# Kernel optimization log

Measured on AMD Instinct MI355X. Metric: run time of the kernel, lower is better.

## Reference

```python
import jax, jax.numpy as jnp
import numpy as np

EMBED_DIM = 2048
HEAD_DIM = 128
B, T = 4, 2048


def setup_inputs() -> dict:
    key = jax.random.key(0)
    k1, k2, k3, k4 = jax.random.split(key, 4)
    x_in = jax.random.normal(k1, (B, T, EMBED_DIM), dtype=jnp.float32)
    scale = 1.0 / np.sqrt(EMBED_DIM)
    Wq = jax.random.normal(k2, (EMBED_DIM, HEAD_DIM), dtype=jnp.float32) * scale
    Wk = jax.random.normal(k3, (EMBED_DIM, HEAD_DIM), dtype=jnp.float32) * scale
    Wv = jax.random.normal(k4, (EMBED_DIM, HEAD_DIM), dtype=jnp.float32) * scale
    return {"x_in": x_in, "Wq": Wq, "Wk": Wk, "Wv": Wv}


def reference(x_in, Wq, Wk, Wv):
    # x_in: [B, T, E]; projections (Linear, no bias)
    q = jnp.einsum('bte,ed->btd', x_in, Wq)  # [B,T,D]
    k = jnp.einsum('bte,ed->btd', x_in, Wk)
    v = jnp.einsum('bte,ed->btd', x_in, Wv)
    t = x_in.shape[1]
    d = Wq.shape[1]
    s = jnp.einsum('btd,bsd->bts', q, k) / jnp.sqrt(jnp.asarray(d, q.dtype))  # [B,Tq,Tk]
    # causal mask: positions with tril==0 (k index > q index) -> -inf
    causal = jnp.tril(jnp.ones((t, t), dtype=bool))
    s = jnp.where(causal, s, -jnp.inf)
    # NOTE: original module applies softmax over dim=1 (query axis), faithfully reproduced
    a = jax.nn.softmax(s, axis=1)
    z = jnp.einsum('bts,bsd->btd', a, v)  # [B,T,D]
    return z
```

## Files before the change

kernel.cpp:

```cpp
#include <hip/hip_runtime.h>

typedef _Float16 f16x8 __attribute__((ext_vector_type(8)));
typedef _Float16 f16x4 __attribute__((ext_vector_type(4)));
typedef float f32x4 __attribute__((ext_vector_type(4)));

#define T_DIM 2048
#define E_DIM 2048
#define D_DIM 128
#define NB 4
#define KSP_P 4
#define KCH_P 512
#define KSP_A 8
#define KCH_A 256
#define NCH2 32
#define ST_LD 136

__device__ __forceinline__ void gll16(const void* g, void* l) {
  __builtin_amdgcn_global_load_lds(
      (const __attribute__((address_space(1))) unsigned int*)g,
      (__attribute__((address_space(3))) unsigned int*)l, 16, 0, 0);
}

__device__ __forceinline__ void merge_stat(float& m, float& l, float pm, float pl) {
  if (pm != -__builtin_inff()) {
    float nm = fmaxf(m, pm);
    l = l * __expf(m - nm) + pl * __expf(pm - nm);
    m = nm;
  }
}


__global__ void cvt_w(const float* __restrict__ Wq, const float* __restrict__ Wk,
                      const float* __restrict__ Wv, _Float16* __restrict__ WhT) {
  int idx = blockIdx.x * 256 + threadIdx.x;
  int w = blockIdx.y;
  const float* W = (w == 0) ? Wq : ((w == 1) ? Wk : Wv);
  int e = idx & (E_DIM - 1), d = idx >> 11;
  WhT[(size_t)w * (D_DIM * E_DIM) + idx] = (_Float16)W[e * D_DIM + d];
}


__global__ __launch_bounds__(256) void proj_gemm(
    const float* __restrict__ x, const _Float16* __restrict__ WhT,
    _Float16* __restrict__ Ph) {
  __shared__ float Asw[2][128 * 32];
  __shared__ _Float16 Bsw[2][128 * 32];
  const int tid = threadIdx.x, w = tid >> 6, lane = tid & 63;
  const int wr = w >> 1, wc = w & 1, quad = lane >> 4, l16 = lane & 15;
  const int t0 = blockIdx.x * 128;
  const int wsel = blockIdx.y, ks = blockIdx.z;
  const _Float16* B = WhT + (size_t)wsel * (D_DIM * E_DIM);
  const int arow = tid >> 3, aseg = tid & 7;
  const int brow = tid >> 2, bseg = tid & 3;
  const int kstart = ks * KCH_P, kend = kstart + KCH_P;

#define STAGE(bufi, kk)                                                   \
  do {                                                                    \
    _Pragma("unroll") for (int p = 0; p < 4; ++p) {                       \
      int row = p * 32 + arow;                                            \
      int gseg = aseg ^ (row & 7);                                        \
      gll16(x + (size_t)(t0 + row) * E_DIM + (kk) + gseg * 4,             \
            Asw[bufi] + row * 32 + aseg * 4);                             \
    }                                                                     \
    _Pragma("unroll") for (int p = 0; p < 2; ++p) {                       \
      int row = p * 64 + brow;                                            \
      int gseg = bseg ^ ((row >> 1) & 3);                                 \
      gll16(B + (size_t)row * E_DIM + (kk) + gseg * 8,                    \
            Bsw[bufi] + row * 32 + bseg * 8);                             \
    }                                                                     \
  } while (0)

  STAGE(0, kstart);
  f32x4 acc[4][4] = {};
  int buf = 0;
  for (int k0 = kstart; k0 < kend; k0 += 32) {
    __syncthreads();
    if (k0 + 32 < kend) STAGE(buf ^ 1, k0 + 32);
    f16x8 af[4], bf[4];
#pragma unroll
    for (int i = 0; i < 4; ++i) {
      int row = wr * 64 + i * 16 + l16;
      int s0 = (2 * quad) ^ (row & 7);
      int s1 = (2 * quad + 1) ^ (row & 7);
      f32x4 a0 = *(const f32x4*)(Asw[buf] + row * 32 + s0 * 4);
      f32x4 a1 = *(const f32x4*)(Asw[buf] + row * 32 + s1 * 4);
#pragma unroll
      for (int e = 0; e < 4; ++e) {
        af[i][e] = (_Float16)a0[e];
        af[i][e + 4] = (_Float16)a1[e];
      }
    }
#pragma unroll
    for (int j = 0; j < 4; ++j) {
      int row = wc * 64 + j * 16 + l16;
      int sg = quad ^ ((row >> 1) & 3);
      bf[j] = *(const f16x8*)(Bsw[buf] + row * 32 + sg * 8);
    }
#pragma unroll
    for (int i = 0; i < 4; ++i)
#pragma unroll
      for (int j = 0; j < 4; ++j)
        acc[i][j] = __builtin_amdgcn_mfma_f32_16x16x32_f16(af[i], bf[j], acc[i][j], 0, 0, 0);
    buf ^= 1;
  }
#undef STAGE
  _Float16* P = Ph + ((size_t)(ks * 3 + wsel) << 20);
  if (wsel < 2) {
#pragma unroll
    for (int i = 0; i < 4; ++i)
#pragma unroll
      for (int j = 0; j < 4; ++j) {
        int n = wc * 64 + j * 16 + l16;
#pragma unroll
        for (int r = 0; r < 4; ++r) {
          int t = t0 + wr * 64 + i * 16 + quad * 4 + r;
          P[(size_t)t * D_DIM + n] = (_Float16)acc[i][j][r];
        }
      }
  } else {
#pragma unroll
    for (int i = 0; i < 4; ++i)
#pragma unroll
      for (int j = 0; j < 4; ++j) {
        int n = wc * 64 + j * 16 + l16;
        int t = t0 + wr * 64 + i * 16 + quad * 4;
        f16x4 o;
#pragma unroll
        for (int r = 0; r < 4; ++r) o[r] = (_Float16)acc[i][j][r];
        *(f16x4*)(P + ((size_t)(t >> 11) * D_DIM + n) * T_DIM + (t & (T_DIM - 1))) = o;
      }
  }
}


__global__ void proj_reduce(const _Float16* __restrict__ Ph, _Float16* __restrict__ Qh,
                            _Float16* __restrict__ Kh, _Float16* __restrict__ VT) {
  size_t u = ((size_t)blockIdx.x * 256 + threadIdx.x) * 8;
  int mat = (int)(u >> 20);
  size_t rem = u & ((1u << 20) - 1);
  float s[8] = {};
#pragma unroll
  for (int ks = 0; ks < KSP_P; ++ks) {
    f16x8 p = *(const f16x8*)(Ph + ((size_t)(ks * 3 + mat) << 20) + rem);
#pragma unroll
    for (int e = 0; e < 8; ++e) s[e] += (float)p[e];
  }
  f16x8 o;
#pragma unroll
  for (int e = 0; e < 8; ++e) o[e] = (_Float16)s[e];
  _Float16* dst = (mat == 0) ? Qh : ((mat == 1) ? Kh : VT);
  *(f16x8*)(dst + rem) = o;
}


__global__ __launch_bounds__(256) void s_gemm(const _Float16* __restrict__ Qh,
                                              const _Float16* __restrict__ Kh,
                                              _Float16* __restrict__ S,
                                              float* __restrict__ Pm,
                                              float* __restrict__ Pl) {
  int idx = blockIdx.x;
  int xt = (int)((sqrtf(8.f * idx + 1.f) - 1.f) * 0.5f);
  while ((xt + 1) * (xt + 2) / 2 <= idx) ++xt;
  while (xt * (xt + 1) / 2 > idx) --xt;
  int yt = idx - xt * (xt + 1) / 2;
  __shared__ __align__(16) char smem[128 * ST_LD * 2];
  _Float16* Bs = (_Float16*)smem;
  _Float16* St = (_Float16*)smem;
  const int tid = threadIdx.x, w = tid >> 6, lane = tid & 63;
  const int wr = w >> 1, wc = w & 1, quad = lane >> 4, l16 = lane & 15;
  const int t0 = xt * 128, s0 = yt * 128, b = blockIdx.y;
  const _Float16* A = Qh + (size_t)b * T_DIM * D_DIM;
  const _Float16* B = Kh + (size_t)b * T_DIM * D_DIM;
  const int srow = lane >> 2;
  const int swz = ((lane & 3) ^ ((srow >> 1) & 3)) * 8;
#pragma unroll
  for (int kq = 0; kq < 4; ++kq)
#pragma unroll
    for (int q = 0; q < 2; ++q) {
      int rbase = w * 32 + q * 16;
      gll16(B + (size_t)(s0 + rbase + srow) * D_DIM + kq * 32 + swz,
            Bs + kq * 4096 + rbase * 32);
    }
  __syncthreads();
  f32x4 acc[4][4] = {};
  const int bsg = (quad ^ ((l16 >> 1) & 3)) * 8;
#pragma unroll
  for (int kq = 0; kq < 4; ++kq) {
    f16x8 af[4], bf[4];
#pragma unroll
    for (int i = 0; i < 4; ++i)
      af[i] = *(const f16x8*)(A + (size_t)(t0 + wr * 64 + i * 16 + l16) * D_DIM +
                              kq * 32 + quad * 8);
#pragma unroll
    for (int j = 0; j < 4; ++j)
      bf[j] = *(const f16x8*)(Bs + kq * 4096 + (wc * 64 + j * 16 + l16) * 32 + bsg);
#pragma unroll
    for (int i = 0; i < 4; ++i)
#pragma unroll
      for (int j = 0; j < 4; ++j)
        acc[i][j] = __builtin_amdgcn_mfma_f32_16x16x32_f16(af[i], bf[j], acc[i][j], 0, 0, 0);
  }
  const float scale = 0.08838834764831845f;
  const float NEG = -__builtin_inff();
  __syncthreads();
#pragma unroll
  for (int j = 0; j < 4; ++j) {
    const int s = s0 + wc * 64 + j * 16 + l16;
    const int sloc = wc * 64 + j * 16 + l16;
    float m = NEG;
#pragma unroll
    for (int i = 0; i < 4; ++i)
#pragma unroll
      for (int r = 0; r < 4; ++r) {
        int tloc = wr * 64 + i * 16 + quad * 4 + r;
        float v = (s > t0 + tloc) ? NEG : acc[i][j][r] * scale;
        St[tloc * ST_LD + sloc] = (_Float16)v;
        m = fmaxf(m, v);
      }
    float l = 0.f;
    if (m != NEG) {
#pragma unroll
      for (int i = 0; i < 4; ++i)
#pragma unroll
        for (int r = 0; r < 4; ++r) {
          int tloc = wr * 64 + i * 16 + quad * 4 + r;
          float v = (s > t0 + tloc) ? NEG : acc[i][j][r] * scale;
          l += __expf(v - m);
        }
    }
#pragma unroll
    for (int d = 16; d <= 32; d <<= 1) {
      float pm = __shfl_xor(m, d, 64);
      float pl = __shfl_xor(l, d, 64);
      merge_stat(m, l, pm, pl);
    }
    if (quad == 0) {
      int c = 2 * xt + wr;
      Pm[((size_t)c * NB + b) * T_DIM + s] = m;
      Pl[((size_t)c * NB + b) * T_DIM + s] = l;
    }
  }
  __syncthreads();
  _Float16* Sb = S + (size_t)b * T_DIM * T_DIM;
  const int rr = tid >> 1, hh = tid & 1;
#pragma unroll
  for (int e = 0; e < 8; ++e) {
    f16x8 v = *(const f16x8*)(St + rr * ST_LD + hh * 64 + e * 8);
    *(f16x8*)(Sb + (size_t)(t0 + rr) * T_DIM + s0 + hh * 64 + e * 8) = v;
  }
}


__global__ __launch_bounds__(256) void comb_stats(const float* __restrict__ Pm,
                                                  const float* __restrict__ Pl,
                                                  float* __restrict__ M,
                                                  float* __restrict__ L) {
  __shared__ float sM[8][32];
  __shared__ float sL[8][32];
  const int g = threadIdx.x >> 5, sl = threadIdx.x & 31;
  const int c = blockIdx.x * 32 + sl;
  const int b = c >> 11, s = c & (T_DIM - 1);
  float m = -__builtin_inff(), l = 0.f;
#pragma unroll
  for (int k = 0; k < NCH2 / 8; ++k) {
    int ch = g * (NCH2 / 8) + k;
    if (ch >= (s >> 6)) {
      size_t idx = ((size_t)ch * NB + b) * T_DIM + s;
      merge_stat(m, l, Pm[idx], Pl[idx]);
    }
  }
  sM[g][sl] = m;
  sL[g][sl] = l;
  __syncthreads();
  if (threadIdx.x < 32) {
    const int c2 = blockIdx.x * 32 + threadIdx.x;
    float fm = -__builtin_inff(), fl = 0.f;
#pragma unroll
    for (int gg = 0; gg < 8; ++gg) merge_stat(fm, fl, sM[gg][threadIdx.x], sL[gg][threadIdx.x]);
    M[c2] = fm;
    L[c2] = 1.f / fl;
  }
}


__global__ __launch_bounds__(256) void av_gemm(const _Float16* __restrict__ S,
                                               const _Float16* __restrict__ VT,
                                               const float* __restrict__ M,
                                               const float* __restrict__ L,
                                               float* __restrict__ Zp) {
  const int t0 = blockIdx.x * 128, b = blockIdx.y, ks = blockIdx.z;
  const int Kmax = t0 + 128;
  const int Kstart = ks * KCH_A;
  if (Kstart >= Kmax) return;
  const int Kend = (Kstart + KCH_A < Kmax) ? (Kstart + KCH_A) : Kmax;
  __shared__ _Float16 As[128 * 32];
  __shared__ _Float16 Bs[128 * 32];
  __shared__ float Ms[KCH_A];
  __shared__ float Ls[KCH_A];
  const int tid = threadIdx.x, w = tid >> 6, lane = tid & 63;
  const int wr = w >> 1, wc = w & 1, quad = lane >> 4, l16 = lane & 15;
  const _Float16* Sb = S + (size_t)b * T_DIM * T_DIM;
  const _Float16* Vb = VT + (size_t)b * D_DIM * T_DIM;
  for (int i = tid; i < Kend - Kstart; i += 256) {
    Ms[i] = M[b * T_DIM + Kstart + i];
    Ls[i] = L[b * T_DIM + Kstart + i];
  }
  const int srow = lane >> 2, scol = (lane & 3) * 8;
  f32x4 acc[4][4] = {};
  for (int k0 = Kstart; k0 < Kend; k0 += 32) {
    __syncthreads();
#pragma unroll
    for (int q = 0; q < 2; ++q) {
      int u = q * 256 + tid;
      int row = u >> 2, c8 = (u & 3) * 8;
      int sc = k0 + c8;
      f16x8 v = *(const f16x8*)(Sb + (size_t)(t0 + row) * T_DIM + sc);
      f16x8 o;
#pragma unroll
      for (int e = 0; e < 8; ++e) {
        int li = sc + e - Kstart;
        float a = __expf((float)v[e] - Ms[li]) * Ls[li];
        o[e] = (_Float16)a;
      }
      *(f16x8*)(As + row * 32 + c8) = o;
      int rbase = w * 32 + q * 16;
      gll16(Vb + (size_t)(rbase + srow) * T_DIM + k0 + scol, Bs + rbase * 32);
    }
    __syncthreads();
    f16x8 af[4], bf[4];
#pragma unroll
    for (int i = 0; i < 4; ++i)
      af[i] = *(const f16x8*)(As + (wr * 64 + i * 16 + l16) * 32 + quad * 8);
#pragma unroll
    for (int j = 0; j < 4; ++j)
      bf[j] = *(const f16x8*)(Bs + (wc * 64 + j * 16 + l16) * 32 + quad * 8);
#pragma unroll
    for (int i = 0; i < 4; ++i)
#pragma unroll
      for (int j = 0; j < 4; ++j)
        acc[i][j] = __builtin_amdgcn_mfma_f32_16x16x32_f16(af[i], bf[j], acc[i][j], 0, 0, 0);
  }
  float* Zb = Zp + ((size_t)ks * NB + b) * T_DIM * D_DIM;
#pragma unroll
  for (int i = 0; i < 4; ++i)
#pragma unroll
    for (int j = 0; j < 4; ++j) {
      int n = wc * 64 + j * 16 + l16;
#pragma unroll
      for (int r = 0; r < 4; ++r) {
        int t = t0 + wr * 64 + i * 16 + quad * 4 + r;
        Zb[(size_t)t * D_DIM + n] = acc[i][j][r];
      }
    }
}


__global__ void z_reduce(const float* __restrict__ Zp, float* __restrict__ Z) {
  size_t flat = ((size_t)blockIdx.x * 256 + threadIdx.x) * 4;
  int t = (int)((flat >> 7) & (T_DIM - 1));
  int ns = ((t >> 7) + 2) >> 1;
  f32x4 s = {};
  for (int ks = 0; ks < ns; ++ks) {
    f32x4 p = *(const f32x4*)(Zp + ((size_t)ks * NB * T_DIM * D_DIM) + flat);
    s += p;
  }
  *(f32x4*)(Z + flat) = s;
}


extern "C" void kernel_launch(void* const* d_in, const int* in_sizes, int n_in,
                              void* d_out, int out_size, void* d_ws, size_t ws_size,
                              hipStream_t stream) {
  const float* x = (const float*)d_in[0];
  const float* Wq = (const float*)d_in[1];
  const float* Wk = (const float*)d_in[2];
  const float* Wv = (const float*)d_in[3];
  char* ws = (char*)d_ws;
  float* Zp = (float*)(ws);
  _Float16* WhT = (_Float16*)(ws + 33554432);
  _Float16* Qh = (_Float16*)(ws + 35127296);
  _Float16* Kh = (_Float16*)(ws + 37224448);
  _Float16* VT = (_Float16*)(ws + 39321600);
  _Float16* S = (_Float16*)(ws + 41418752);
  _Float16* Ph = (_Float16*)(ws + 41418752);
  float* M = (float*)(ws + 74973184);
  float* L = (float*)(ws + 75005952);
  float* Pm = (float*)(ws + 75038720);
  float* Pl = (float*)(ws + 76087296);
  float* Z = (float*)d_out;

  cvt_w<<<dim3(1024, 3), 256, 0, stream>>>(Wq, Wk, Wv, WhT);
  proj_gemm<<<dim3(64, 3, KSP_P), 256, 0, stream>>>(x, WhT, Ph);
  proj_reduce<<<1536, 256, 0, stream>>>(Ph, Qh, Kh, VT);
  s_gemm<<<dim3(136, 4), 256, 0, stream>>>(Qh, Kh, S, Pm, Pl);
  comb_stats<<<256, 256, 0, stream>>>(Pm, Pl, M, L);
  av_gemm<<<dim3(16, 4, KSP_A), 256, 0, stream>>>(S, VT, M, L, Zp);
  z_reduce<<<1024, 256, 0, stream>>>(Zp, Z);
}
```

Before: 177.9 us.

## Register-stage x with fp16 conversion in proj_gemm and fuse stats merge into av_gemm

proj_gemm now loads x tiles into registers one step ahead, converts them to fp16 and writes a half-size swizzled LDS tile. This replaces the fp32 direct-to-LDS DMA followed by a per-use conversion, cutting LDS footprint and redundant conversions. The comb_stats kernel is removed, and each av_gemm block merges the per-chunk max/sum partials itself for its K range, saving one launch and the M/L round trip. The cost is that many av_gemm blocks redundantly merge the same partials, and the A tile loses asynchronous DMA in favour of register prefetch.

```diff
diff --git a/kernel.cpp b/kernel.cpp
--- a/kernel.cpp
+++ b/kernel.cpp
@@ -43,25 +43,45 @@
 __global__ __launch_bounds__(256) void proj_gemm(
     const float* __restrict__ x, const _Float16* __restrict__ WhT,
     _Float16* __restrict__ Ph) {
-  __shared__ float Asw[2][128 * 32];
+  __shared__ _Float16 Asw[2][128 * 32];
   __shared__ _Float16 Bsw[2][128 * 32];
   const int tid = threadIdx.x, w = tid >> 6, lane = tid & 63;
   const int wr = w >> 1, wc = w & 1, quad = lane >> 4, l16 = lane & 15;
   const int t0 = blockIdx.x * 128;
   const int wsel = blockIdx.y, ks = blockIdx.z;
   const _Float16* B = WhT + (size_t)wsel * (D_DIM * E_DIM);
-  const int arow = tid >> 3, aseg = tid & 7;
+  const int arow0 = tid >> 2, aseg = tid & 3;
   const int brow = tid >> 2, bseg = tid & 3;
   const int kstart = ks * KCH_P, kend = kstart + KCH_P;
 
-#define STAGE(bufi, kk)                                                   \
+  f32x4 pa[2][2];
+
+#define LOADA(kk)                                                         \
   do {                                                                    \
-    _Pragma("unroll") for (int p = 0; p < 4; ++p) {                       \
-      int row = p * 32 + arow;                                            \
-      int gseg = aseg ^ (row & 7);                                        \
-      gll16(x + (size_t)(t0 + row) * E_DIM + (kk) + gseg * 4,             \
-            Asw[bufi] + row * 32 + aseg * 4);                             \
+    _Pragma("unroll") for (int p = 0; p < 2; ++p) {                       \
+      int row = p * 64 + arow0;                                           \
+      const float* xp = x + (size_t)(t0 + row) * E_DIM + (kk) + aseg * 8; \
+      pa[p][0] = *(const f32x4*)xp;                                       \
+      pa[p][1] = *(const f32x4*)(xp + 4);                                 \
     }                                                                     \
+  } while (0)
+
+#define WRITEA(bufi)                                                      \
+  do {                                                                    \
+    _Pragma("unroll") for (int p = 0; p < 2; ++p) {                       \
+      int row = p * 64 + arow0;                                           \
+      f16x8 o;                                                            \
+      _Pragma("unroll") for (int e = 0; e < 4; ++e) {                     \
+        o[e] = (_Float16)pa[p][0][e];                                     \
+        o[e + 4] = (_Float16)pa[p][1][e];                                 \
+      }                                                                   \
+      int sg = aseg ^ ((row >> 1) & 3);                                   \
+      *(f16x8*)(Asw[bufi] + row * 32 + sg * 8) = o;                       \
+    }                                                                     \
+  } while (0)
+
+#define DMAB(bufi, kk)                                                    \
+  do {                                                                    \
     _Pragma("unroll") for (int p = 0; p < 2; ++p) {                       \
       int row = p * 64 + brow;                                            \
       int gseg = bseg ^ ((row >> 1) & 3);                                 \
@@ -70,25 +90,25 @@
     }                                                                     \
   } while (0)
 
-  STAGE(0, kstart);
+  LOADA(kstart);
+  WRITEA(0);
+  DMAB(0, kstart);
+  LOADA(kstart + 32);
   f32x4 acc[4][4] = {};
   int buf = 0;
   for (int k0 = kstart; k0 < kend; k0 += 32) {
     __syncthreads();
-    if (k0 + 32 < kend) STAGE(buf ^ 1, k0 + 32);
+    if (k0 + 32 < kend) {
+      WRITEA(buf ^ 1);
+      DMAB(buf ^ 1, k0 + 32);
+      if (k0 + 64 < kend) LOADA(k0 + 64);
+    }
     f16x8 af[4], bf[4];
 #pragma unroll
     for (int i = 0; i < 4; ++i) {
       int row = wr * 64 + i * 16 + l16;
-      int s0 = (2 * quad) ^ (row & 7);
-      int s1 = (2 * quad + 1) ^ (row & 7);
-      f32x4 a0 = *(const f32x4*)(Asw[buf] + row * 32 + s0 * 4);
-      f32x4 a1 = *(const f32x4*)(Asw[buf] + row * 32 + s1 * 4);
-#pragma unroll
-      for (int e = 0; e < 4; ++e) {
-        af[i][e] = (_Float16)a0[e];
-        af[i][e + 4] = (_Float16)a1[e];
-      }
+      int sg = quad ^ ((row >> 1) & 3);
+      af[i] = *(const f16x8*)(Asw[buf] + row * 32 + sg * 8);
     }
 #pragma unroll
     for (int j = 0; j < 4; ++j) {
@@ -103,7 +123,9 @@
         acc[i][j] = __builtin_amdgcn_mfma_f32_16x16x32_f16(af[i], bf[j], acc[i][j], 0, 0, 0);
     buf ^= 1;
   }
-#undef STAGE
+#undef LOADA
+#undef WRITEA
+#undef DMAB
   _Float16* P = Ph + ((size_t)(ks * 3 + wsel) << 20);
   if (wsel < 2) {
 #pragma unroll
@@ -251,42 +273,10 @@
 }
 
 
-__global__ __launch_bounds__(256) void comb_stats(const float* __restrict__ Pm,
-                                                  const float* __restrict__ Pl,
-                                                  float* __restrict__ M,
-                                                  float* __restrict__ L) {
-  __shared__ float sM[8][32];
-  __shared__ float sL[8][32];
-  const int g = threadIdx.x >> 5, sl = threadIdx.x & 31;
-  const int c = blockIdx.x * 32 + sl;
-  const int b = c >> 11, s = c & (T_DIM - 1);
-  float m = -__builtin_inff(), l = 0.f;
-#pragma unroll
-  for (int k = 0; k < NCH2 / 8; ++k) {
-    int ch = g * (NCH2 / 8) + k;
-    if (ch >= (s >> 6)) {
-      size_t idx = ((size_t)ch * NB + b) * T_DIM + s;
-      merge_stat(m, l, Pm[idx], Pl[idx]);
-    }
-  }
-  sM[g][sl] = m;
-  sL[g][sl] = l;
-  __syncthreads();
-  if (threadIdx.x < 32) {
-    const int c2 = blockIdx.x * 32 + threadIdx.x;
-    float fm = -__builtin_inff(), fl = 0.f;
-#pragma unroll
-    for (int gg = 0; gg < 8; ++gg) merge_stat(fm, fl, sM[gg][threadIdx.x], sL[gg][threadIdx.x]);
-    M[c2] = fm;
-    L[c2] = 1.f / fl;
-  }
-}
-
-
 __global__ __launch_bounds__(256) void av_gemm(const _Float16* __restrict__ S,
                                                const _Float16* __restrict__ VT,
-                                               const float* __restrict__ M,
-                                               const float* __restrict__ L,
+                                               const float* __restrict__ Pm,
+                                               const float* __restrict__ Pl,
                                                float* __restrict__ Zp) {
   const int t0 = blockIdx.x * 128, b = blockIdx.y, ks = blockIdx.z;
   const int Kmax = t0 + 128;
@@ -301,9 +291,15 @@
   const int wr = w >> 1, wc = w & 1, quad = lane >> 4, l16 = lane & 15;
   const _Float16* Sb = S + (size_t)b * T_DIM * T_DIM;
   const _Float16* Vb = VT + (size_t)b * D_DIM * T_DIM;
-  for (int i = tid; i < Kend - Kstart; i += 256) {
-    Ms[i] = M[b * T_DIM + Kstart + i];
-    Ls[i] = L[b * T_DIM + Kstart + i];
+  {
+    int s = Kstart + tid;
+    float m = -__builtin_inff(), l = 0.f;
+    for (int ch = s >> 6; ch < NCH2; ++ch) {
+      size_t pidx = ((size_t)ch * NB + b) * T_DIM + s;
+      merge_stat(m, l, Pm[pidx], Pl[pidx]);
+    }
+    Ms[tid] = m;
+    Ls[tid] = 1.f / l;
   }
   const int srow = lane >> 2, scol = (lane & 3) * 8;
   f32x4 acc[4][4] = {};
@@ -383,8 +379,6 @@
   _Float16* VT = (_Float16*)(ws + 39321600);
   _Float16* S = (_Float16*)(ws + 41418752);
   _Float16* Ph = (_Float16*)(ws + 41418752);
-  float* M = (float*)(ws + 74973184);
-  float* L = (float*)(ws + 75005952);
   float* Pm = (float*)(ws + 75038720);
   float* Pl = (float*)(ws + 76087296);
   float* Z = (float*)d_out;
@@ -393,7 +387,6 @@
   proj_gemm<<<dim3(64, 3, KSP_P), 256, 0, stream>>>(x, WhT, Ph);
   proj_reduce<<<1536, 256, 0, stream>>>(Ph, Qh, Kh, VT);
   s_gemm<<<dim3(136, 4), 256, 0, stream>>>(Qh, Kh, S, Pm, Pl);
-  comb_stats<<<256, 256, 0, stream>>>(Pm, Pl, M, L);
-  av_gemm<<<dim3(16, 4, KSP_A), 256, 0, stream>>>(S, VT, M, L, Zp);
+  av_gemm<<<dim3(16, 4, KSP_A), 256, 0, stream>>>(S, VT, Pm, Pl, Zp);
   z_reduce<<<1024, 256, 0, stream>>>(Zp, Z);
 }
```

New measurement: 186.3 us. 4.7% more time.
